# Performance work log

Measured on AMD Instinct MI355X. Metric: run time of the kernel, lower is better.

The kernel has to match this reference:

```python
import jax, jax.numpy as jnp
import numpy as np

B, C, W, H = 16, 512, 64, 64
OUT, NH = 512, 8
HD = OUT // NH          # 64
K = 64                  # kernel_size == attended axis length (height)


def setup_inputs() -> dict:
    key = jax.random.key(0)
    k0, k1, k2, k3 = jax.random.split(key, 4)
    s = float(HD) ** -0.5
    return {
        "x": jax.random.normal(k0, (B, C, W, H), jnp.float32),
        "in_proj_weight": jax.random.normal(k1, (2 * OUT, C), jnp.float32) * s,
        "in_proj_bias": jnp.zeros((2 * OUT,), jnp.float32),
        "out_proj_w": jax.random.normal(k2, (OUT, OUT), jnp.float32) * s,
        "out_proj_b": jnp.zeros((OUT,), jnp.float32),
        "relative": jax.random.normal(k3, (2 * HD, 2 * K - 1), jnp.float32) * s,
    }


def reference(x, in_proj_weight, in_proj_bias, out_proj_w, out_proj_b, relative):
    b, c, w, h = x.shape
    hd2 = HD // 2
    # width=False, self-attention path: permute(0,3,2,1) then flat view
    xq = jnp.transpose(x, (0, 3, 2, 1)).reshape(b * w, h, c)
    qkv = xq @ in_proj_weight.T + in_proj_bias
    q, k, v = jnp.split(qkv, [OUT // 2, OUT], axis=2)

    # relative position embeddings gathered into [2*HD, K, K]
    rel_idx = jnp.arange(K)[:, None] - jnp.arange(K)[None, :] + (K - 1)  # key i, query j
    emb = relative[:, rel_idx]                                          # [2*HD, K, K]
    q_emb, k_emb, v_emb = jnp.split(emb, [hd2, HD], axis=0)

    # [bw, heads, ch, pos]
    q = q.reshape(b * w, h, NH, hd2).transpose(0, 2, 3, 1)
    k = k.reshape(b * w, h, NH, hd2).transpose(0, 2, 3, 1)
    v = v.reshape(b * w, h, NH, HD).transpose(0, 2, 3, 1)

    qr = jnp.einsum('bgci,cij->bgij', q, q_emb)
    kr = jnp.einsum('bgci,cij->bgij', k, k_emb).swapaxes(2, 3)
    qk = jnp.einsum('bgci,bgcj->bgij', q, k)
    sim = jax.nn.softmax(qk + qr + kr, axis=3)

    sv = jnp.einsum('bgij,bgcj->bgci', sim, v)     # [bw, NH, HD, h]
    sve = jnp.einsum('bgij,cij->bgci', sim, v_emb)  # [bw, NH, HD, h]
    out = (sv + sve).reshape(b * w, OUT, h).swapaxes(1, 2)  # [bw, h, OUT]
    out = out @ out_proj_w.T + out_proj_b
    # [b, w, h, OUT] -> transpose(2,3) -> permute(0,2,3,1) == transpose(0,3,2,1)
    out = out.reshape(b, w, h, OUT).transpose(0, 3, 2, 1)   # [B, OUT, H, W]
    return out
```

## Files before the change

### kernel.cpp

```cpp
#include <hip/hip_runtime.h>

using u16 = unsigned short;
using u32 = unsigned int;
typedef __attribute__((ext_vector_type(8))) _Float16 h8v;
typedef __attribute__((ext_vector_type(8))) u16 us8;
typedef __attribute__((ext_vector_type(2))) u32 u32x2;
typedef __attribute__((ext_vector_type(4))) float f4v;

__device__ __forceinline__ u16 f2h(float f) {
  _Float16 h = (_Float16)f;
  return __builtin_bit_cast(unsigned short, h);
}
__device__ __forceinline__ _Float16 bits2h(u16 u) {
  return __builtin_bit_cast(_Float16, u);
}

__device__ __forceinline__ f4v mfma16(h8v a, h8v b, f4v c) {
  return __builtin_amdgcn_mfma_f32_16x16x32_f16(a, b, c, 0, 0, 0);
}

__device__ __forceinline__ void gll16(const void* g, void* l) {
  __builtin_amdgcn_global_load_lds(
      (const __attribute__((address_space(1))) void*)g,
      (__attribute__((address_space(3))) void*)l, 16, 0, 0);
}


__global__ __launch_bounds__(256) void k0_setup(
    const float* __restrict__ w1, const float* __restrict__ wout,
    const float* __restrict__ rel, u16* __restrict__ W1b, u16* __restrict__ Woutb,
    u16* __restrict__ EqT, u16* __restrict__ EkT, u16* __restrict__ Evp)
{
  int idx = blockIdx.x * 256 + threadIdx.x;
  if (idx < 524288) {
    W1b[idx] = f2h(w1[idx]);
  } else if (idx < 786432) {
    int k = idx - 524288; Woutb[k] = f2h(wout[k]);
  } else if (idx < 790528) {
    int k = idx - 786432; int t = k >> 5, c = k & 31;
    EqT[k] = (t < 127) ? f2h(rel[c * 127 + t]) : (u16)0;
  } else if (idx < 794624) {
    int k = idx - 790528; int t = k >> 5, c = k & 31;
    EkT[k] = (t < 127) ? f2h(rel[(32 + c) * 127 + t]) : (u16)0;
  } else if (idx < 802816) {
    int k = idx - 794624; int c = k >> 7, t = k & 127;
    Evp[k] = (t < 127) ? f2h(rel[(64 + c) * 127 + t]) : (u16)0;
  }
}

__global__ __launch_bounds__(256, 2) void k1_qkv(
    const float* __restrict__ x, const u16* __restrict__ W1b,
    const float* __restrict__ bias, u16* __restrict__ qkv)
{
  __shared__ u16 POOL[40960];
  u16* XL = POOL;
  u16* WD = POOL + 32768;
  const int bid = blockIdx.x;
  const int b = bid >> 6, w = bid & 63;
  const int tid = threadIdx.x;
  const int l = tid & 63, wv = tid >> 6;
  const int lr = l & 15, lg = l >> 4;
  const int osub = (wv & 1) * 64;
  const int rsub = (wv >> 1) * 32;

  auto stageB = [&](int ot, int kk, int buf) {
#pragma unroll
    for (int q = 0; q < 2; q++) {
      int slot = q * 256 + tid;
      int o = slot >> 2, c4 = slot & 3;
      gll16(W1b + (size_t)(ot * 128 + o) * 512 + kk * 32 +
                ((c4 ^ ((o >> 1) & 3)) << 3),
            WD + buf * 4096 + slot * 8);
    }
  };

  stageB(0, 0, 0);

  {
    const int r = tid & 63;
    const int cb = tid >> 6;
    const float* xb = x + ((size_t)b * 512 * 64 + w) * 64 + r;
#pragma unroll
    for (int q = 0; q < 16; q++) {
      int cc = (q << 2) | cb;
      float v[8];
#pragma unroll
      for (int e = 0; e < 8; e++)
        v[e] = xb[(size_t)(cc * 8 + e) * 4096];
      us8 o;
#pragma unroll
      for (int e = 0; e < 8; e++) o[e] = f2h(v[e]);
      *(us8*)&XL[r * 512 + ((cc ^ (r & 7)) << 3)] = o;
    }
  }
  __syncthreads();

  for (int ot = 0; ot < 8; ot++) {
    const int o0 = ot * 128;
    f4v acc[4][2];
#pragma unroll
    for (int mt = 0; mt < 4; mt++)
#pragma unroll
      for (int nt = 0; nt < 2; nt++) acc[mt][nt] = (f4v){0.f, 0.f, 0.f, 0.f};

#pragma unroll
    for (int kk = 0; kk < 16; kk++) {
      int cur = kk & 1;
      if (kk < 15) stageB(ot, kk + 1, cur ^ 1);
      h8v wf[4], xf[2];
#pragma unroll
      for (int mt = 0; mt < 4; mt++) {
        int o = osub + mt * 16 + lr;
        wf[mt] = *(const h8v*)&WD[cur * 4096 + o * 32 +
                                  ((lg ^ ((o >> 1) & 3)) << 3)];
      }
#pragma unroll
      for (int nt = 0; nt < 2; nt++) {
        int r = rsub + nt * 16 + lr;
        int cc = kk * 4 + lg;
        xf[nt] = *(const h8v*)&XL[r * 512 + ((cc ^ (r & 7)) << 3)];
      }
#pragma unroll
      for (int mt = 0; mt < 4; mt++)
#pragma unroll
        for (int nt = 0; nt < 2; nt++)
          acc[mt][nt] = mfma16(wf[mt], xf[nt], acc[mt][nt]);
      __syncthreads();
    }

    u16* Tr = WD;
    float4 bias4[4];
#pragma unroll
    for (int mt = 0; mt < 4; mt++)
      bias4[mt] = *(const float4*)&bias[o0 + osub + mt * 16 + lg * 4];
#pragma unroll
    for (int mt = 0; mt < 4; mt++)
#pragma unroll
      for (int nt = 0; nt < 2; nt++) {
        int r = rsub + nt * 16 + lr;
#pragma unroll
        for (int ep = 0; ep < 2; ep++) {
          int o_ = osub + mt * 16 + lg * 4 + 2 * ep;
          float v0 = acc[mt][nt][2 * ep + 0] + ((const float*)&bias4[mt])[2 * ep + 0];
          float v1 = acc[mt][nt][2 * ep + 1] + ((const float*)&bias4[mt])[2 * ep + 1];
          unsigned pk = (unsigned)f2h(v0) | ((unsigned)f2h(v1) << 16);
          int cc = o_ >> 3;
          int dst = (cc & 8) | ((cc & 7) ^ (r & 7));
          *(unsigned*)&Tr[r * 128 + dst * 8 + (o_ & 7)] = pk;
        }
      }
    __syncthreads();
#pragma unroll
    for (int p = 0; p < 4; p++) {
      int u = p * 256 + tid;
      int r = u >> 4, cc = u & 15;
      int dst = (cc & 8) | ((cc & 7) ^ (r & 7));
      us8 v = *(const us8*)&Tr[r * 128 + dst * 8];
      size_t S = (size_t)(b * 64 + r) * 64 + w;
      *(us8*)&qkv[S * 1024 + o0 + cc * 8] = v;
    }
    __syncthreads();
    if (ot < 7) { stageB(ot + 1, 0, 0); __syncthreads(); }
  }
}

__global__ __launch_bounds__(256) void k2_attn(
    const u16* __restrict__ qkv, const u16* __restrict__ EqT,
    const u16* __restrict__ EkT, const u16* __restrict__ Evp,
    u16* __restrict__ attn, int g0)
{
  const int bid = blockIdx.x;
  const int s = bid & 1023, g = g0 + (bid >> 10);
  const int tid = threadIdx.x;
  const int l = tid & 63, wv = tid >> 6;
  const int lr = l & 15, lg = l >> 4;
  const int i0 = wv * 16;
  const u16* base = qkv + (size_t)s * 65536;

  __shared__ __align__(16) u16 POOL[16896];
  u16* QEi = POOL;
  u16* KEj = POOL + 8448;
  u16* Pl  = POOL;
  u16* VTl = POOL + 4096;
  u16* Psh = POOL + 8192;

  us8 vreg0, vreg1;
  {
    int u0 = tid,        j0_ = u0 >> 3, cb0 = u0 & 7;
    int u1 = tid + 256,  j1_ = u1 >> 3, cb1 = u1 & 7;
    vreg0 = *(const us8*)(base + j0_ * 1024 + 512 + g * 64 + cb0 * 8);
    vreg1 = *(const us8*)(base + j1_ * 1024 + 512 + g * 64 + cb1 * 8);
  }

  h8v qf = *(const h8v*)(base + (i0 + lr) * 1024 + g * 32 + lg * 8);
  h8v kf[4];
#pragma unroll
  for (int jt = 0; jt < 4; jt++)
    kf[jt] = *(const h8v*)(base + (jt * 16 + lr) * 1024 + 256 + g * 32 + lg * 8);

  const f4v z4 = {0.f, 0.f, 0.f, 0.f};

#pragma unroll
  for (int tt = 0; tt < 8; tt++) {
    h8v eb = *(const h8v*)(EqT + (tt * 16 + lr) * 32 + lg * 8);
    f4v d = mfma16(eb, qf, z4);
    int tb = tt * 16 + 4 * lg;
    u32x2 pk;
    pk[0] = (u32)f2h(d[0]) | ((u32)f2h(d[1]) << 16);
    pk[1] = (u32)f2h(d[2]) | ((u32)f2h(d[3]) << 16);
    *(u32x2*)&QEi[(i0 + lr) * 132 + tb] = pk;
  }
#pragma unroll
  for (int q = 0; q < 2; q++) {
    int tt = wv * 2 + q;
    h8v ea = *(const h8v*)(EkT + (tt * 16 + lr) * 32 + lg * 8);
#pragma unroll
    for (int jt = 0; jt < 4; jt++) {
      f4v d = mfma16(ea, kf[jt], z4);
      int tb = tt * 16 + 4 * lg;
      u32x2 pk;
      pk[0] = (u32)f2h(d[0]) | ((u32)f2h(d[1]) << 16);
      pk[1] = (u32)f2h(d[2]) | ((u32)f2h(d[3]) << 16);
      *(u32x2*)&KEj[(jt * 16 + lr) * 132 + tb] = pk;
    }
  }
  f4v sc[4];
#pragma unroll
  for (int jt = 0; jt < 4; jt++) sc[jt] = mfma16(kf[jt], qf, z4);

  __syncthreads();

  const int i = i0 + lr;
  float pv[4][4];
  {
    int qbase = i * 133 + 63 - 4 * lg;
    int kbase = 8448 + 4 * lg * 133 + 63 - i;
#pragma unroll
    for (int jt = 0; jt < 4; jt++)
#pragma unroll
      for (int e = 0; e < 4; e++) {
        float qr = (float)bits2h(POOL[qbase - 16 * jt - e]);
        float kr = (float)bits2h(POOL[kbase + 2128 * jt + 133 * e]);
        pv[jt][e] = sc[jt][e] + qr + kr;
      }
  }
  float inv;
  {
    float m = pv[0][0];
#pragma unroll
    for (int jt = 0; jt < 4; jt++)
#pragma unroll
      for (int e = 0; e < 4; e++) m = fmaxf(m, pv[jt][e]);
    m = fmaxf(m, __shfl_xor(m, 16));
    m = fmaxf(m, __shfl_xor(m, 32));
    float t0 = 0.f;
#pragma unroll
    for (int jt = 0; jt < 4; jt++)
#pragma unroll
      for (int e = 0; e < 4; e++) {
        pv[jt][e] = exp2f((pv[jt][e] - m) * 1.4426950408889634f);
        t0 += pv[jt][e];
      }
    t0 += __shfl_xor(t0, 16);
    t0 += __shfl_xor(t0, 32);
    inv = 1.f / t0;
  }
#pragma unroll
  for (int jt = 0; jt < 4; jt++)
#pragma unroll
    for (int e = 0; e < 4; e++) pv[jt][e] *= inv;

  __syncthreads();

#pragma unroll
  for (int jt = 0; jt < 4; jt++) {
    int j0 = jt * 16 + 4 * lg;
    int jc = j0 >> 3;
    u32x2 pk;
    pk[0] = (u32)f2h(pv[jt][0]) | ((u32)f2h(pv[jt][1]) << 16);
    pk[1] = (u32)f2h(pv[jt][2]) | ((u32)f2h(pv[jt][3]) << 16);
    *(u32x2*)&Pl[i * 64 + ((jc ^ (i & 7)) << 3) + (j0 & 7)] = pk;
#pragma unroll
    for (int e = 0; e < 4; e++) {
      int d = i + 63 - (j0 + e);
      int cd = d >> 3;
      Psh[i * 128 + (((cd & 8) | ((cd & 7) ^ (i & 7))) << 3) + (d & 7)] =
          f2h(pv[jt][e]);
    }
  }
  {
    int zi = tid >> 2;
#pragma unroll
    for (int kk = 0; kk < 16; kk++) {
      int k = (tid & 3) * 16 + kk;
      int col = (k < zi) ? k : (k + 64);
      int cd = col >> 3;
      Psh[zi * 128 + (((cd & 8) | ((cd & 7) ^ (zi & 7))) << 3) + (col & 7)] = 0;
    }
    int u0 = tid, j0_ = u0 >> 3, cb0 = u0 & 7;
#pragma unroll
    for (int e = 0; e < 8; e++) {
      int c = cb0 * 8 + e;
      VTl[c * 64 + (((j0_ >> 3) ^ (c & 7)) << 3) + (j0_ & 7)] = (u16)vreg0[e];
    }
    int u1 = tid + 256, j1_ = u1 >> 3, cb1 = u1 & 7;
#pragma unroll
    for (int e = 0; e < 8; e++) {
      int c = cb1 * 8 + e;
      VTl[c * 64 + (((j1_ >> 3) ^ (c & 7)) << 3) + (j1_ & 7)] = (u16)vreg1[e];
    }
  }
  __syncthreads();

  f4v acc[4] = {z4, z4, z4, z4};
  {
#pragma unroll
    for (int kc = 0; kc < 2; kc++) {
      h8v pa = *(const h8v*)&Pl[i * 64 + (((kc * 4 + lg) ^ (i & 7)) << 3)];
#pragma unroll
      for (int ct = 0; ct < 4; ct++) {
        int cA = ct * 16 + lr;
        h8v vb = *(const h8v*)&VTl[cA * 64 + (((kc * 4 + lg) ^ (cA & 7)) << 3)];
        acc[ct] = mfma16(pa, vb, acc[ct]);
      }
    }
#pragma unroll
    for (int tc = 0; tc < 4; tc++) {
      int cd = tc * 4 + lg;
      int cds = (cd & 8) | ((cd & 7) ^ (i & 7));
      h8v pa = *(const h8v*)&Psh[i * 128 + cds * 8];
#pragma unroll
      for (int ct = 0; ct < 4; ct++) {
        h8v eb = *(const h8v*)(Evp + (ct * 16 + lr) * 128 + tc * 32 + lg * 8);
        acc[ct] = mfma16(pa, eb, acc[ct]);
      }
    }
  }
#pragma unroll
  for (int ct = 0; ct < 4; ct++)
#pragma unroll
    for (int r = 0; r < 4; r++) {
      int io = i0 + lg * 4 + r;
      attn[(size_t)(s * 64 + io) * 512 + g * 64 + ct * 16 + lr] = f2h(acc[ct][r]);
    }
}

__global__ __launch_bounds__(512) void k3_oproj(
    const u16* __restrict__ attn, const u16* __restrict__ Woutb,
    const float* __restrict__ ob, float* __restrict__ out)
{
  const int bid = blockIdx.x;
  const int b = bid >> 6, w = bid & 63;
  const int tid = threadIdx.x;
  const int l = tid & 63, wv = tid >> 6;
  const int lr = l & 15, lg = l >> 4;

  __shared__ u16 Bl[2][64 * 64];

  f4v acc[4][4];
#pragma unroll
  for (int a_ = 0; a_ < 4; a_++)
#pragma unroll
    for (int b_ = 0; b_ < 4; b_++) acc[a_][b_] = (f4v){0.f, 0.f, 0.f, 0.f};

  auto stageB = [&](int kk, int buf) {
    int c0 = kk * 64;
    int h_l = wv * 8 + (l >> 3);
    int p = l & 7;
    const u16* src = attn + ((size_t)b * 4096 + (size_t)h_l * 64 + w) * 512 + c0 +
                     ((p ^ (h_l & 7)) << 3);
    gll16(src, &Bl[buf][wv * 512]);
  };

  stageB(0, 0);
  __syncthreads();

  for (int kk = 0; kk < 8; kk++) {
    int cur = kk & 1, nxt = cur ^ 1;
    if (kk < 7) stageB(kk + 1, nxt);
    int c0 = kk * 64;
    h8v af[4][2], bf[4][2];
#pragma unroll
    for (int mt = 0; mt < 4; mt++)
#pragma unroll
      for (int kc = 0; kc < 2; kc++)
        af[mt][kc] = *(const h8v*)(Woutb + (size_t)(wv * 64 + mt * 16 + lr) * 512 +
                                   c0 + kc * 32 + lg * 8);
#pragma unroll
    for (int jt = 0; jt < 4; jt++)
#pragma unroll
      for (int kc = 0; kc < 2; kc++) {
        int h = jt * 16 + lr;
        bf[jt][kc] = *(const h8v*)&Bl[cur][h * 64 + (((kc * 4 + lg) ^ (h & 7)) << 3)];
      }
#pragma unroll
    for (int mt = 0; mt < 4; mt++)
#pragma unroll
      for (int jt = 0; jt < 4; jt++)
#pragma unroll
        for (int kc = 0; kc < 2; kc++)
          acc[mt][jt] = mfma16(af[mt][kc], bf[jt][kc], acc[mt][jt]);
    __syncthreads();
  }

#pragma unroll
  for (int mt = 0; mt < 4; mt++)
#pragma unroll
    for (int jt = 0; jt < 4; jt++)
#pragma unroll
      for (int e = 0; e < 4; e++) {
        int o = wv * 64 + mt * 16 + lg * 4 + e;
        int h = jt * 16 + lr;
        out[(((size_t)b * 512 + o) * 64 + w) * 64 + h] = acc[mt][jt][e] + ob[o];
      }
}

extern "C" void kernel_launch(void* const* d_in, const int* in_sizes, int n_in,
                              void* d_out, int out_size, void* d_ws, size_t ws_size,
                              hipStream_t stream)
{
  (void)in_sizes; (void)n_in; (void)out_size; (void)ws_size;
  const float* x    = (const float*)d_in[0];
  const float* w1   = (const float*)d_in[1];
  const float* b1   = (const float*)d_in[2];
  const float* wout = (const float*)d_in[3];
  const float* bo   = (const float*)d_in[4];
  const float* rel  = (const float*)d_in[5];
  float* out = (float*)d_out;

  char* ws = (char*)d_ws;
  u16* qkv_ws  = (u16*)ws;
  u16* attn_ws = (u16*)(ws + 134217728);
  u16* W1b     = (u16*)(ws + 201326592);
  u16* Woutb   = (u16*)(ws + 202375168);
  u16* EqT     = (u16*)(ws + 202899456);
  u16* EkT     = (u16*)(ws + 202907648);
  u16* Evp     = (u16*)(ws + 202915840);

  k0_setup<<<dim3(3136), dim3(256), 0, stream>>>(w1, wout, rel, W1b, Woutb, EqT, EkT, Evp);
  k1_qkv  <<<dim3(1024), dim3(256), 0, stream>>>(x, W1b, b1, qkv_ws);
  k2_attn <<<dim3(4096), dim3(256), 0, stream>>>(qkv_ws, EqT, EkT, Evp, attn_ws, 0);
  k2_attn <<<dim3(4096), dim3(256), 0, stream>>>(qkv_ws, EqT, EkT, Evp, attn_ws, 4);
  k3_oproj<<<dim3(1024), dim3(512), 0, stream>>>(attn_ws, Woutb, bo, out);
}
```

Before: 336.0 us.

## Stage output-projection weights through LDS with double-buffered async loads

The output projection kernel used to read its fp16 weight tiles straight from global memory into registers on every k-step. It now double-buffers 32-column weight slices in LDS using async global-to-LDS loads with an XOR swizzle, and halves the k-step size to 32. The attention tile staging is also restructured so that all 512 threads issue it once per 64-column pair. This trades more LDS (80KB per block), twice as many barriers and a launch_bounds occupancy hint for hiding weight-load latency behind the MFMA work.

New measurement: 333.8 us. About the same (-0.7%).

```diff
diff --git a/kernel.cpp b/kernel.cpp
--- a/kernel.cpp
+++ b/kernel.cpp
@@ -345,71 +345,79 @@
     }
 }
 
-__global__ __launch_bounds__(512) void k3_oproj(
+__global__ __launch_bounds__(512, 4) void k3_oproj(
     const u16* __restrict__ attn, const u16* __restrict__ Woutb,
     const float* __restrict__ ob, float* __restrict__ out)
 {
+  __shared__ u16 POOL3[40960];
+  u16* WD = POOL3;
+  u16* Bl = POOL3 + 32768;
   const int bid = blockIdx.x;
   const int b = bid >> 6, w = bid & 63;
   const int tid = threadIdx.x;
   const int l = tid & 63, wv = tid >> 6;
   const int lr = l & 15, lg = l >> 4;
-
-  __shared__ u16 Bl[2][64 * 64];
+  const int osub = wv * 64;
+
+  auto stageW = [&](int kk, int buf) {
+#pragma unroll
+    for (int q = 0; q < 4; q++) {
+      int slot = q * 512 + tid;
+      int o = slot >> 2, c4 = slot & 3;
+      gll16(Woutb + (size_t)o * 512 + kk * 32 + ((c4 ^ ((o >> 1) & 3)) << 3),
+            WD + buf * 16384 + slot * 8);
+    }
+  };
+  auto stageA = [&](int pr, int buf) {
+    int h_l = tid >> 3, p = tid & 7;
+    gll16(attn + ((size_t)b * 4096 + (size_t)h_l * 64 + w) * 512 + pr * 64 +
+              ((p ^ (h_l & 7)) << 3),
+          Bl + buf * 4096 + tid * 8);
+  };
+
+  stageW(0, 0);
+  stageA(0, 0);
+  __syncthreads();
 
   f4v acc[4][4];
 #pragma unroll
-  for (int a_ = 0; a_ < 4; a_++)
-#pragma unroll
-    for (int b_ = 0; b_ < 4; b_++) acc[a_][b_] = (f4v){0.f, 0.f, 0.f, 0.f};
-
-  auto stageB = [&](int kk, int buf) {
-    int c0 = kk * 64;
-    int h_l = wv * 8 + (l >> 3);
-    int p = l & 7;
-    const u16* src = attn + ((size_t)b * 4096 + (size_t)h_l * 64 + w) * 512 + c0 +
-                     ((p ^ (h_l & 7)) << 3);
-    gll16(src, &Bl[buf][wv * 512]);
-  };
-
-  stageB(0, 0);
-  __syncthreads();
-
-  for (int kk = 0; kk < 8; kk++) {
-    int cur = kk & 1, nxt = cur ^ 1;
-    if (kk < 7) stageB(kk + 1, nxt);
-    int c0 = kk * 64;
-    h8v af[4][2], bf[4][2];
+  for (int mt = 0; mt < 4; mt++)
+#pragma unroll
+    for (int jt = 0; jt < 4; jt++) acc[mt][jt] = (f4v){0.f, 0.f, 0.f, 0.f};
+
+  for (int kk = 0; kk < 16; kk++) {
+    int curW = kk & 1;
+    int pr = kk >> 1, curA = pr & 1;
+    if (kk < 15) stageW(kk + 1, curW ^ 1);
+    if ((kk & 1) == 0 && pr < 7) stageA(pr + 1, curA ^ 1);
+    h8v af[4], bf[4];
+#pragma unroll
+    for (int mt = 0; mt < 4; mt++) {
+      int o = osub + mt * 16 + lr;
+      af[mt] = *(const h8v*)&WD[curW * 16384 + o * 32 +
+                                ((lg ^ ((o >> 1) & 3)) << 3)];
+    }
+#pragma unroll
+    for (int jt = 0; jt < 4; jt++) {
+      int h = jt * 16 + lr;
+      bf[jt] = *(const h8v*)&Bl[curA * 4096 + h * 64 +
+                                ((((kk & 1) * 4 + lg) ^ (h & 7)) << 3)];
+    }
 #pragma unroll
     for (int mt = 0; mt < 4; mt++)
 #pragma unroll
-      for (int kc = 0; kc < 2; kc++)
-        af[mt][kc] = *(const h8v*)(Woutb + (size_t)(wv * 64 + mt * 16 + lr) * 512 +
-                                   c0 + kc * 32 + lg * 8);
+      for (int jt = 0; jt < 4; jt++)
+        acc[mt][jt] = mfma16(af[mt], bf[jt], acc[mt][jt]);
+    __syncthreads();
+  }
+
+#pragma unroll
+  for (int mt = 0; mt < 4; mt++)
 #pragma unroll
     for (int jt = 0; jt < 4; jt++)
 #pragma unroll
-      for (int kc = 0; kc < 2; kc++) {
-        int h = jt * 16 + lr;
-        bf[jt][kc] = *(const h8v*)&Bl[cur][h * 64 + (((kc * 4 + lg) ^ (h & 7)) << 3)];
-      }
-#pragma unroll
-    for (int mt = 0; mt < 4; mt++)
-#pragma unroll
-      for (int jt = 0; jt < 4; jt++)
-#pragma unroll
-        for (int kc = 0; kc < 2; kc++)
-          acc[mt][jt] = mfma16(af[mt][kc], bf[jt][kc], acc[mt][jt]);
-    __syncthreads();
-  }
-
-#pragma unroll
-  for (int mt = 0; mt < 4; mt++)
-#pragma unroll
-    for (int jt = 0; jt < 4; jt++)
-#pragma unroll
       for (int e = 0; e < 4; e++) {
-        int o = wv * 64 + mt * 16 + lg * 4 + e;
+        int o = osub + mt * 16 + lg * 4 + e;
         int h = jt * 16 + lr;
         out[(((size_t)b * 512 + o) * 64 + w) * 64 + h] = acc[mt][jt][e] + ob[o];
       }
```
